# Kernel optimization log

Hardware: AMD Instinct MI355X
Metric: run time of the kernel (lower is better)

The kernel has to match this reference:

```python
import jax, jax.numpy as jnp
import numpy as np
from jax.scipy.linalg import expm as _expm

# --- hyperparameters from transop_cfg ---
LAMBDA_PRIOR = 0.05      # L1 weight (cfg.lambda_prior)
FISTA_ITERS = 20         # cfg.fista_num_iterations
FISTA_LR = 0.01          # FISTA step size
PSI_SCALE = 0.01         # stable operator initialization scale

B, D, K, M, N = 256, 512, 8, 64, 64  # batch, feat dim, blocks, dict size, block dim


def _batch_expm(T):
    # T: [B, K, N, N] -> expm applied to each NxN matrix
    Bk = T.shape[0] * T.shape[1]
    Texp = jax.vmap(_expm)(T.reshape(Bk, N, N))
    return Texp.reshape(T.shape)


def transop_apply(z0, c, psi):
    """z1_hat = expm(sum_m c_m psi[k,m]) @ z0_block, block-diagonal over K blocks.
    z0: [B, D], c: [B, M], psi: [K, M, N, N] -> [B, D]
    """
    z0b = z0.reshape(z0.shape[0], K, N)                  # [B, K, N]
    T = jnp.einsum('bm,kmuv->bkuv', c, psi)              # [B, K, N, N]
    Texp = _batch_expm(T)
    z1b = jnp.einsum('bkuv,bkv->bku', Texp, z0b)         # [B, K, N]
    return z1b.reshape(z0.shape)


def _soft_threshold(x, thr):
    return jnp.sign(x) * jnp.maximum(jnp.abs(x) - thr, 0.0)


def infer_coefficients(z0, z1, psi):
    """FISTA for min_c 0.5*||expm(c.psi) z0 - z1||^2 + lambda*||c||_1."""
    def smooth_loss(c):
        z1_hat = transop_apply(z0, c, psi)
        return 0.5 * jnp.sum((z1_hat - z1) ** 2)

    grad_fn = jax.grad(smooth_loss)

    def body(carry, _):
        c, y, t = carry
        g = grad_fn(y)
        c_new = _soft_threshold(y - FISTA_LR * g, FISTA_LR * LAMBDA_PRIOR)
        t_new = 0.5 * (1.0 + jnp.sqrt(1.0 + 4.0 * t * t))
        y_new = c_new + ((t - 1.0) / t_new) * (c_new - c)
        return (c_new, y_new, t_new), None

    c0 = jnp.zeros((z0.shape[0], M), dtype=z0.dtype)
    (c, _, _), _ = jax.lax.scan(body, (c0, c0, jnp.float32(1.0)), None, length=FISTA_ITERS)
    return c


def setup_inputs() -> dict:
    key = jax.random.key(0)
    k0, k1, kp = jax.random.split(key, 3)
    feature_0 = jax.random.normal(k0, (B, D), dtype=jnp.float32)
    feature_1 = jax.random.normal(k1, (B, D), dtype=jnp.float32)
    psi = PSI_SCALE * jax.random.normal(kp, (K, M, N, N), dtype=jnp.float32)
    return {"feature_0": feature_0, "feature_1": feature_1, "psi": psi}


def reference(feature_0, feature_1, psi):
    z0, z1 = feature_0, feature_1
    # Coefficients inferred on detached features/operators (z0.detach(), psi.float())
    c = infer_coefficients(jax.lax.stop_gradient(z0),
                           jax.lax.stop_gradient(z1),
                           jax.lax.stop_gradient(psi))
    c = jax.lax.stop_gradient(c)
    # Transport: z1_hat = transop(z0, c) with grads flowing to z0 and psi
    z1_hat = transop_apply(z0, c, psi)
    return z1_hat
```

## Files before the change

kernel.cpp:

```cpp
#include <hip/hip_runtime.h>
#include <hip/hip_bf16.h>


typedef __attribute__((ext_vector_type(8))) short bf16x8;
typedef __attribute__((ext_vector_type(4))) float f32x4;
typedef unsigned short ushort_t;
typedef unsigned int uint_t;

__device__ __constant__ float INVF[20] = {
    1.0f, 1.0f, 0.5f, 1.6666666666666666e-1f, 4.1666666666666664e-2f,
    8.333333333333333e-3f, 1.3888888888888889e-3f, 1.984126984126984e-4f,
    2.48015873015873e-5f, 2.7557319223985893e-6f, 2.755731922398589e-7f,
    2.505210838544172e-8f, 2.08767569878681e-9f, 1.6059043836821613e-10f,
    1.1470745597729725e-11f, 7.647163731819816e-13f, 4.779477332387385e-14f,
    2.8114572543455206e-15f, 1.5619206968586225e-16f, 8.22063524662433e-18f};

__device__ __forceinline__ ushort_t f2b(float x) {
    uint_t u = __float_as_uint(x);
    uint_t r = u + 0x7FFFu + ((u >> 16) & 1u);
    return (ushort_t)(r >> 16);
}
__device__ __forceinline__ float b2f(ushort_t h) {
    return __uint_as_float((uint_t)h << 16);
}

__device__ __forceinline__ float qsum4(float s) {
    int a = __builtin_amdgcn_update_dpp(0, __float_as_int(s), 0xB1, 0xF, 0xF, true);
    s += __int_as_float(a);
    int b = __builtin_amdgcn_update_dpp(0, __float_as_int(s), 0x4E, 0xF, 0xF, true);
    s += __int_as_float(b);
    return s;
}

__global__ __launch_bounds__(256) void prep_k(const float* __restrict__ psi,
                                              ushort_t* __restrict__ psiB,
                                              ushort_t* __restrict__ psiT,
                                              uint4* __restrict__ zero_base) {
    if (blockIdx.x < 48)
        zero_base[blockIdx.x * 256 + threadIdx.x] = make_uint4(0, 0, 0, 0);
    int base = blockIdx.x * 2048 + threadIdx.x;
    for (int i = 0; i < 8; ++i) {
        int e = base + i * 256;
        float v = psi[e];
        ushort_t h = f2b(v);
        psiB[e] = h;
        int k = e >> 18;
        int r = e & 262143;
        int m = r >> 12;
        int uv = r & 4095;
        psiT[(size_t)k * 262144 + (size_t)uv * 64 + m] = h;
    }
}

__global__ __launch_bounds__(256) void gemm1_k(const ushort_t* __restrict__ ybf,
                                               const ushort_t* __restrict__ psiT,
                                               ushort_t* __restrict__ Tbf) {
    __shared__ __align__(16) ushort_t Ls[128 * 72];
    int wg = blockIdx.x;
    int j0 = (wg & 511) * 64;
    int bt = wg >> 9;
    int tid = threadIdx.x;
    int wave = tid >> 6, lane = tid & 63;
    int rowi = lane & 15, q = lane >> 4;
    int b0w = bt * 128 + wave * 32;

    f32x4 acc[4][2];
    const f32x4 zero = {0.f, 0.f, 0.f, 0.f};
    for (int ta = 0; ta < 4; ++ta)
        for (int tb = 0; tb < 2; ++tb) acc[ta][tb] = zero;

    for (int ks = 0; ks < 2; ++ks) {
        bf16x8 a[4], bb[2];
        for (int ta = 0; ta < 4; ++ta)
            a[ta] = *(const bf16x8*)(psiT + (size_t)(j0 + ta * 16 + rowi) * 64 +
                                     ks * 32 + q * 8);
        for (int tb = 0; tb < 2; ++tb)
            bb[tb] = *(const bf16x8*)(ybf + (size_t)(b0w + tb * 16 + rowi) * 64 +
                                      ks * 32 + q * 8);
        for (int ta = 0; ta < 4; ++ta)
            for (int tb = 0; tb < 2; ++tb)
                acc[ta][tb] = __builtin_amdgcn_mfma_f32_16x16x32_bf16(
                    a[ta], bb[tb], acc[ta][tb], 0, 0, 0);
    }
    for (int ta = 0; ta < 4; ++ta)
        for (int tb = 0; tb < 2; ++tb) {
            int bl = wave * 32 + tb * 16 + rowi;
            int jl = ta * 16 + q * 4;
            uint_t lo = (uint_t)f2b(acc[ta][tb][0]) | ((uint_t)f2b(acc[ta][tb][1]) << 16);
            uint_t hi = (uint_t)f2b(acc[ta][tb][2]) | ((uint_t)f2b(acc[ta][tb][3]) << 16);
            int idx = bl * 72 + ((((jl >> 3) + 2 * bl) & 7) << 3) + (jl & 7);
            *(uint2*)&Ls[idx] = make_uint2(lo, hi);
        }
    __syncthreads();
    for (int pass = 0; pass < 4; ++pass) {
        int b = pass * 32 + (tid >> 3);
        int ch = tid & 7;
        uint4 v = *(const uint4*)&Ls[b * 72 + ch * 8];
        int x = (ch - 2 * b) & 7;
        *(uint4*)(Tbf + (size_t)(bt * 128 + b) * 32768 + j0 + x * 8) = v;
    }
}

template <int NT>
__global__ __launch_bounds__(256) void krylov_k(ushort_t* __restrict__ Tbf,
                                                const float* __restrict__ z0,
                                                const float* __restrict__ z1,
                                                float* __restrict__ out) {
    __shared__ float V[NT][64];
    __shared__ float U[NT][64];
    __shared__ float zz[64];
    int bid = blockIdx.x;
    int b = bid >> 3, k = bid & 7;
    int tid = threadIdx.x;
    int row = tid >> 2, p = tid & 3, c0 = p * 16;
    bool grad = (out == nullptr);

    const ushort_t* tbase = Tbf + (size_t)bid * 4096;
    float rowT[16];
    {
        uint4 ra = *(const uint4*)(tbase + row * 64 + c0);
        uint4 rb = *(const uint4*)(tbase + row * 64 + c0 + 8);
        uint_t wv[8] = {ra.x, ra.y, ra.z, ra.w, rb.x, rb.y, rb.z, rb.w};
        for (int i = 0; i < 8; ++i) {
            rowT[2 * i]     = __uint_as_float(wv[i] << 16);
            rowT[2 * i + 1] = __uint_as_float(wv[i] & 0xFFFF0000u);
        }
    }
    float colT[16];
    if (grad) {
#pragma unroll
        for (int i = 0; i < 16; ++i) colT[i] = b2f(tbase[(c0 + i) * 64 + row]);
    }
    if (tid < 64) {
        V[0][tid] = z0[(size_t)b * 512 + k * 64 + tid];
        zz[tid]   = z1[(size_t)b * 512 + k * 64 + tid];
    }
    __syncthreads();

    for (int l = 1; l < NT; ++l) {
        const f32x4* vp = (const f32x4*)&V[l - 1][c0];
        f32x4 v0 = vp[0], v1 = vp[1], v2 = vp[2], v3 = vp[3];
        float s0 = 0.f, s1 = 0.f, s2 = 0.f, s3 = 0.f;
#pragma unroll
        for (int i = 0; i < 4; ++i) {
            s0 = fmaf(rowT[i], v0[i], s0);
            s1 = fmaf(rowT[4 + i], v1[i], s1);
            s2 = fmaf(rowT[8 + i], v2[i], s2);
            s3 = fmaf(rowT[12 + i], v3[i], s3);
        }
        float s = qsum4((s0 + s1) + (s2 + s3));
        if (p == 0) V[l][row] = s;
        __syncthreads();
    }

    if (!grad) {
        if (tid < 64) {
            float zh = 0.f;
#pragma unroll
            for (int l = 0; l < NT; ++l) zh = fmaf(INVF[l], V[l][tid], zh);
            out[(size_t)b * 512 + k * 64 + tid] = zh;
        }
        return;
    }

    if (tid < 64) {
        float zh = 0.f;
#pragma unroll
        for (int l = 0; l < NT; ++l) zh = fmaf(INVF[l], V[l][tid], zh);
        U[0][tid] = zh - zz[tid];
    }
    __syncthreads();

    for (int j = 1; j < NT; ++j) {
        const f32x4* up = (const f32x4*)&U[j - 1][c0];
        f32x4 u0 = up[0], u1 = up[1], u2 = up[2], u3 = up[3];
        float s0 = 0.f, s1 = 0.f, s2 = 0.f, s3 = 0.f;
#pragma unroll
        for (int i = 0; i < 4; ++i) {
            s0 = fmaf(colT[i], u0[i], s0);
            s1 = fmaf(colT[4 + i], u1[i], s1);
            s2 = fmaf(colT[8 + i], u2[i], s2);
            s3 = fmaf(colT[12 + i], u3[i], s3);
        }
        float s = qsum4((s0 + s1) + (s2 + s3));
        if (p == 0) U[j][row] = s;
        __syncthreads();
    }

    float W[NT];
#pragma unroll
    for (int l = 0; l < NT; ++l) {
        float w = 0.f;
#pragma unroll
        for (int j = 0; j < NT; ++j) w = fmaf(INVF[j + l + 1], U[j][row], w);
        W[l] = w;
    }
    float o[16];
#pragma unroll
    for (int i = 0; i < 16; ++i) o[i] = 0.f;
#pragma unroll
    for (int l = 0; l < NT; ++l) {
        const f32x4* vp = (const f32x4*)&V[l][c0];
        f32x4 a0 = vp[0], a1 = vp[1], a2 = vp[2], a3 = vp[3];
        float w = W[l];
#pragma unroll
        for (int i = 0; i < 4; ++i) {
            o[i]      = fmaf(w, a0[i], o[i]);
            o[4 + i]  = fmaf(w, a1[i], o[4 + i]);
            o[8 + i]  = fmaf(w, a2[i], o[8 + i]);
            o[12 + i] = fmaf(w, a3[i], o[12 + i]);
        }
    }
    uint_t ow[8];
#pragma unroll
    for (int i = 0; i < 8; ++i)
        ow[i] = (uint_t)f2b(o[2 * i]) | ((uint_t)f2b(o[2 * i + 1]) << 16);
    uint4* op = (uint4*)(Tbf + (size_t)bid * 4096 + row * 64 + c0);
    op[0] = make_uint4(ow[0], ow[1], ow[2], ow[3]);
    op[1] = make_uint4(ow[4], ow[5], ow[6], ow[7]);
}

__global__ __launch_bounds__(256) void gemm2_k(const ushort_t* __restrict__ Obf,
                                               const ushort_t* __restrict__ psiB,
                                               float* __restrict__ gpart) {
    __shared__ __align__(16) float Lg[64 * 68];
    int bt = blockIdx.x & 3;
    int kc = blockIdx.x >> 2;
    int k = kc >> 3;
    int uv0 = (kc & 7) * 512;
    int tid = threadIdx.x, wave = tid >> 6, lane = tid & 63;
    int rowi = lane & 15, q = lane >> 4;

    f32x4 acc[4][4];
    const f32x4 zero = {0.f, 0.f, 0.f, 0.f};
    for (int ta = 0; ta < 4; ++ta)
        for (int tb = 0; tb < 4; ++tb) acc[ta][tb] = zero;

    for (int ks = 0; ks < 4; ++ks) {
        int off = uv0 + wave * 128 + ks * 32 + q * 8;
        bf16x8 a[4], bb[4];
        for (int ta = 0; ta < 4; ++ta)
            a[ta] = *(const bf16x8*)(psiB + (size_t)k * 262144 +
                                     (size_t)(ta * 16 + rowi) * 4096 + off);
        for (int tb = 0; tb < 4; ++tb)
            bb[tb] = *(const bf16x8*)(Obf +
                                      (size_t)(bt * 64 + tb * 16 + rowi) * 32768 +
                                      k * 4096 + off);
        for (int ta = 0; ta < 4; ++ta)
            for (int tb = 0; tb < 4; ++tb)
                acc[ta][tb] = __builtin_amdgcn_mfma_f32_16x16x32_bf16(
                    a[ta], bb[tb], acc[ta][tb], 0, 0, 0);
    }
    for (int w = 0; w < 4; ++w) {
        if (wave == w) {
            for (int ta = 0; ta < 4; ++ta)
                for (int tb = 0; tb < 4; ++tb) {
                    float* dst = &Lg[(tb * 16 + rowi) * 68 + ta * 16 + q * 4];
                    if (w == 0) *(f32x4*)dst = acc[ta][tb];
                    else {
                        f32x4 t = *(const f32x4*)dst;
                        t += acc[ta][tb];
                        *(f32x4*)dst = t;
                    }
                }
        }
        __syncthreads();
    }
    int b = tid >> 2, mq = tid & 3;
    float* gp = gpart + (size_t)kc * 16384 + (size_t)(bt * 64 + b) * 64 + mq * 16;
    const float* lp = &Lg[b * 68 + mq * 16];
    for (int i = 0; i < 4; ++i)
        *(f32x4*)(gp + 4 * i) = *(const f32x4*)(lp + 4 * i);
}

__global__ __launch_bounds__(256) void fista_update(const float* __restrict__ gpart,
                                                    float* __restrict__ cb,
                                                    float* __restrict__ yb,
                                                    ushort_t* __restrict__ cbf,
                                                    ushort_t* __restrict__ ybf,
                                                    int iter) {
    int idx = blockIdx.x * 256 + threadIdx.x;
    float a0 = 0.f, a1 = 0.f, a2 = 0.f, a3 = 0.f;
#pragma unroll
    for (int p = 0; p < 64; p += 4) {
        a0 += gpart[(size_t)p * 16384 + idx];
        a1 += gpart[(size_t)(p + 1) * 16384 + idx];
        a2 += gpart[(size_t)(p + 2) * 16384 + idx];
        a3 += gpart[(size_t)(p + 3) * 16384 + idx];
    }
    float gv = (a0 + a1) + (a2 + a3);
    float t = 1.f;
    for (int s = 0; s < iter; ++s) t = 0.5f * (1.f + sqrtf(1.f + 4.f * t * t));
    float tn = 0.5f * (1.f + sqrtf(1.f + 4.f * t * t));
    float beta = (t - 1.f) / tn;
    float co = cb[idx], yo = yb[idx];
    float a = yo - 0.01f * gv;
    float thr = 0.01f * 0.05f;
    float cn = copysignf(fmaxf(fabsf(a) - thr, 0.f), a);
    float yn = cn + beta * (cn - co);
    cb[idx] = cn;
    yb[idx] = yn;
    cbf[idx] = f2b(cn);
    ybf[idx] = f2b(yn);
}

extern "C" void kernel_launch(void* const* d_in, const int* in_sizes, int n_in,
                              void* d_out, int out_size, void* d_ws, size_t ws_size,
                              hipStream_t stream) {
    const float* z0 = (const float*)d_in[0];
    const float* z1 = (const float*)d_in[1];
    const float* psi = (const float*)d_in[2];
    float* out = (float*)d_out;

    char* w = (char*)d_ws;
    ushort_t* TO    = (ushort_t*)(w);
    ushort_t* psiB  = (ushort_t*)(w + 16777216);
    ushort_t* psiT  = (ushort_t*)(w + 20971520);
    float*    gpart = (float*)(w + 25165824);
    float*    cbuf  = (float*)(w + 29360128);
    float*    ybuf  = (float*)(w + 29425664);
    ushort_t* cbf   = (ushort_t*)(w + 29491200);
    ushort_t* ybf   = (ushort_t*)(w + 29523968);

    prep_k<<<1024, 256, 0, stream>>>(psi, psiB, psiT, (uint4*)(w + 29360128));

    for (int it = 0; it < 20; ++it) {
        gemm1_k<<<1024, 256, 0, stream>>>(ybf, psiT, TO);
        krylov_k<5><<<2048, 256, 0, stream>>>(TO, z0, z1, nullptr);
        gemm2_k<<<256, 256, 0, stream>>>(TO, psiB, gpart);
        fista_update<<<64, 256, 0, stream>>>(gpart, cbuf, ybuf, cbf, ybf, it);
    }

    gemm1_k<<<1024, 256, 0, stream>>>(cbf, psiT, TO);
    krylov_k<8><<<2048, 256, 0, stream>>>(TO, z0, z1, out);
}
```

Baseline: 844.1 us.

## Map one wave per Krylov matrix with register-resident rows and readlane broadcasts

Each 64x64 Krylov matrix is now handled by a single wave instead of a whole 256-thread block. Each lane holds a full row (and column) of T in registers, and vector elements are broadcast with readlane, which removes the shared-memory round trips and block-wide barriers at every Krylov step. The gemm2 reduction also changes: each wave writes its partial tile to its own LDS slice and one sync precedes a combined sum, replacing four serialized sync rounds. The cost is very high register pressure (64-element rowT/colT/o arrays), which lowers occupancy and risks spills, and the strided column load is uncoalesced.

```diff
diff --git a/kernel.cpp b/kernel.cpp
--- a/kernel.cpp
+++ b/kernel.cpp
@@ -23,13 +23,8 @@
 __device__ __forceinline__ float b2f(ushort_t h) {
     return __uint_as_float((uint_t)h << 16);
 }
-
-__device__ __forceinline__ float qsum4(float s) {
-    int a = __builtin_amdgcn_update_dpp(0, __float_as_int(s), 0xB1, 0xF, 0xF, true);
-    s += __int_as_float(a);
-    int b = __builtin_amdgcn_update_dpp(0, __float_as_int(s), 0x4E, 0xF, 0xF, true);
-    s += __int_as_float(b);
-    return s;
+__device__ __forceinline__ float rdlane(float v, int l) {
+    return __int_as_float(__builtin_amdgcn_readlane(__float_as_int(v), l));
 }
 
 __global__ __launch_bounds__(256) void prep_k(const float* __restrict__ psi,
@@ -101,129 +96,112 @@
     }
 }
 
-template <int NT>
+template <int NT, int GRAD>
 __global__ __launch_bounds__(256) void krylov_k(ushort_t* __restrict__ Tbf,
                                                 const float* __restrict__ z0,
                                                 const float* __restrict__ z1,
                                                 float* __restrict__ out) {
-    __shared__ float V[NT][64];
-    __shared__ float U[NT][64];
-    __shared__ float zz[64];
-    int bid = blockIdx.x;
+    int lane = threadIdx.x & 63;
+    int bid = blockIdx.x * 4 + (threadIdx.x >> 6);
     int b = bid >> 3, k = bid & 7;
-    int tid = threadIdx.x;
-    int row = tid >> 2, p = tid & 3, c0 = p * 16;
-    bool grad = (out == nullptr);
-
-    const ushort_t* tbase = Tbf + (size_t)bid * 4096;
-    float rowT[16];
+    ushort_t* tbase = Tbf + (size_t)bid * 4096;
+
+    float rowT[64];
     {
-        uint4 ra = *(const uint4*)(tbase + row * 64 + c0);
-        uint4 rb = *(const uint4*)(tbase + row * 64 + c0 + 8);
-        uint_t wv[8] = {ra.x, ra.y, ra.z, ra.w, rb.x, rb.y, rb.z, rb.w};
-        for (int i = 0; i < 8; ++i) {
-            rowT[2 * i]     = __uint_as_float(wv[i] << 16);
-            rowT[2 * i + 1] = __uint_as_float(wv[i] & 0xFFFF0000u);
-        }
-    }
-    float colT[16];
-    if (grad) {
-#pragma unroll
-        for (int i = 0; i < 16; ++i) colT[i] = b2f(tbase[(c0 + i) * 64 + row]);
-    }
-    if (tid < 64) {
-        V[0][tid] = z0[(size_t)b * 512 + k * 64 + tid];
-        zz[tid]   = z1[(size_t)b * 512 + k * 64 + tid];
-    }
-    __syncthreads();
-
+        const uint4* tp = (const uint4*)(tbase + (size_t)lane * 64);
+#pragma unroll
+        for (int cc = 0; cc < 8; ++cc) {
+            uint4 v = tp[cc];
+            uint_t w[4] = {v.x, v.y, v.z, v.w};
+#pragma unroll
+            for (int i = 0; i < 4; ++i) {
+                rowT[cc * 8 + 2 * i]     = __uint_as_float(w[i] << 16);
+                rowT[cc * 8 + 2 * i + 1] = __uint_as_float(w[i] & 0xFFFF0000u);
+            }
+        }
+    }
+
+    float vs[NT];
+    vs[0] = z0[(size_t)b * 512 + k * 64 + lane];
+#pragma unroll
     for (int l = 1; l < NT; ++l) {
-        const f32x4* vp = (const f32x4*)&V[l - 1][c0];
-        f32x4 v0 = vp[0], v1 = vp[1], v2 = vp[2], v3 = vp[3];
-        float s0 = 0.f, s1 = 0.f, s2 = 0.f, s3 = 0.f;
-#pragma unroll
-        for (int i = 0; i < 4; ++i) {
-            s0 = fmaf(rowT[i], v0[i], s0);
-            s1 = fmaf(rowT[4 + i], v1[i], s1);
-            s2 = fmaf(rowT[8 + i], v2[i], s2);
-            s3 = fmaf(rowT[12 + i], v3[i], s3);
-        }
-        float s = qsum4((s0 + s1) + (s2 + s3));
-        if (p == 0) V[l][row] = s;
-        __syncthreads();
-    }
-
-    if (!grad) {
-        if (tid < 64) {
-            float zh = 0.f;
-#pragma unroll
-            for (int l = 0; l < NT; ++l) zh = fmaf(INVF[l], V[l][tid], zh);
-            out[(size_t)b * 512 + k * 64 + tid] = zh;
-        }
+        float sp = vs[l - 1];
+        float a0 = 0.f, a1 = 0.f, a2 = 0.f, a3 = 0.f;
+#pragma unroll
+        for (int i = 0; i < 64; i += 4) {
+            a0 = fmaf(rowT[i],     rdlane(sp, i),     a0);
+            a1 = fmaf(rowT[i + 1], rdlane(sp, i + 1), a1);
+            a2 = fmaf(rowT[i + 2], rdlane(sp, i + 2), a2);
+            a3 = fmaf(rowT[i + 3], rdlane(sp, i + 3), a3);
+        }
+        vs[l] = (a0 + a1) + (a2 + a3);
+    }
+
+    float zh = 0.f;
+#pragma unroll
+    for (int l = 0; l < NT; ++l) zh = fmaf(INVF[l], vs[l], zh);
+
+    if constexpr (!GRAD) {
+        out[(size_t)b * 512 + k * 64 + lane] = zh;
         return;
-    }
-
-    if (tid < 64) {
-        float zh = 0.f;
-#pragma unroll
-        for (int l = 0; l < NT; ++l) zh = fmaf(INVF[l], V[l][tid], zh);
-        U[0][tid] = zh - zz[tid];
-    }
-    __syncthreads();
-
-    for (int j = 1; j < NT; ++j) {
-        const f32x4* up = (const f32x4*)&U[j - 1][c0];
-        f32x4 u0 = up[0], u1 = up[1], u2 = up[2], u3 = up[3];
-        float s0 = 0.f, s1 = 0.f, s2 = 0.f, s3 = 0.f;
-#pragma unroll
-        for (int i = 0; i < 4; ++i) {
-            s0 = fmaf(colT[i], u0[i], s0);
-            s1 = fmaf(colT[4 + i], u1[i], s1);
-            s2 = fmaf(colT[8 + i], u2[i], s2);
-            s3 = fmaf(colT[12 + i], u3[i], s3);
-        }
-        float s = qsum4((s0 + s1) + (s2 + s3));
-        if (p == 0) U[j][row] = s;
-        __syncthreads();
-    }
-
-    float W[NT];
-#pragma unroll
-    for (int l = 0; l < NT; ++l) {
-        float w = 0.f;
-#pragma unroll
-        for (int j = 0; j < NT; ++j) w = fmaf(INVF[j + l + 1], U[j][row], w);
-        W[l] = w;
-    }
-    float o[16];
-#pragma unroll
-    for (int i = 0; i < 16; ++i) o[i] = 0.f;
-#pragma unroll
-    for (int l = 0; l < NT; ++l) {
-        const f32x4* vp = (const f32x4*)&V[l][c0];
-        f32x4 a0 = vp[0], a1 = vp[1], a2 = vp[2], a3 = vp[3];
-        float w = W[l];
-#pragma unroll
-        for (int i = 0; i < 4; ++i) {
-            o[i]      = fmaf(w, a0[i], o[i]);
-            o[4 + i]  = fmaf(w, a1[i], o[4 + i]);
-            o[8 + i]  = fmaf(w, a2[i], o[8 + i]);
-            o[12 + i] = fmaf(w, a3[i], o[12 + i]);
-        }
-    }
-    uint_t ow[8];
-#pragma unroll
-    for (int i = 0; i < 8; ++i)
-        ow[i] = (uint_t)f2b(o[2 * i]) | ((uint_t)f2b(o[2 * i + 1]) << 16);
-    uint4* op = (uint4*)(Tbf + (size_t)bid * 4096 + row * 64 + c0);
-    op[0] = make_uint4(ow[0], ow[1], ow[2], ow[3]);
-    op[1] = make_uint4(ow[4], ow[5], ow[6], ow[7]);
+    } else {
+        float colT[64];
+#pragma unroll
+        for (int i = 0; i < 64; ++i)
+            colT[i] = b2f(tbase[(size_t)i * 64 + lane]);
+
+        float us[NT];
+        us[0] = zh - z1[(size_t)b * 512 + k * 64 + lane];
+#pragma unroll
+        for (int j = 1; j < NT; ++j) {
+            float sp = us[j - 1];
+            float a0 = 0.f, a1 = 0.f, a2 = 0.f, a3 = 0.f;
+#pragma unroll
+            for (int i = 0; i < 64; i += 4) {
+                a0 = fmaf(colT[i],     rdlane(sp, i),     a0);
+                a1 = fmaf(colT[i + 1], rdlane(sp, i + 1), a1);
+                a2 = fmaf(colT[i + 2], rdlane(sp, i + 2), a2);
+                a3 = fmaf(colT[i + 3], rdlane(sp, i + 3), a3);
+            }
+            us[j] = (a0 + a1) + (a2 + a3);
+        }
+
+        float W[NT];
+#pragma unroll
+        for (int l = 0; l < NT; ++l) {
+            float w = 0.f;
+#pragma unroll
+            for (int j = 0; j < NT; ++j) w = fmaf(INVF[j + l + 1], us[j], w);
+            W[l] = w;
+        }
+
+        float o[64];
+#pragma unroll
+        for (int c = 0; c < 64; ++c) o[c] = 0.f;
+#pragma unroll
+        for (int l = 0; l < NT; ++l) {
+            float wl = W[l];
+#pragma unroll
+            for (int c = 0; c < 64; ++c)
+                o[c] = fmaf(wl, rdlane(vs[l], c), o[c]);
+        }
+
+        uint4* op = (uint4*)(tbase + (size_t)lane * 64);
+#pragma unroll
+        for (int cc = 0; cc < 8; ++cc) {
+            uint_t w0 = (uint_t)f2b(o[cc * 8 + 0]) | ((uint_t)f2b(o[cc * 8 + 1]) << 16);
+            uint_t w1 = (uint_t)f2b(o[cc * 8 + 2]) | ((uint_t)f2b(o[cc * 8 + 3]) << 16);
+            uint_t w2 = (uint_t)f2b(o[cc * 8 + 4]) | ((uint_t)f2b(o[cc * 8 + 5]) << 16);
+            uint_t w3 = (uint_t)f2b(o[cc * 8 + 6]) | ((uint_t)f2b(o[cc * 8 + 7]) << 16);
+            op[cc] = make_uint4(w0, w1, w2, w3);
+        }
+    }
 }
 
 __global__ __launch_bounds__(256) void gemm2_k(const ushort_t* __restrict__ Obf,
                                                const ushort_t* __restrict__ psiB,
                                                float* __restrict__ gpart) {
-    __shared__ __align__(16) float Lg[64 * 68];
+    __shared__ __align__(16) float Lg[4][64 * 68];
     int bt = blockIdx.x & 3;
     int kc = blockIdx.x >> 2;
     int k = kc >> 3;
@@ -251,26 +229,24 @@
                 acc[ta][tb] = __builtin_amdgcn_mfma_f32_16x16x32_bf16(
                     a[ta], bb[tb], acc[ta][tb], 0, 0, 0);
     }
-    for (int w = 0; w < 4; ++w) {
-        if (wave == w) {
-            for (int ta = 0; ta < 4; ++ta)
-                for (int tb = 0; tb < 4; ++tb) {
-                    float* dst = &Lg[(tb * 16 + rowi) * 68 + ta * 16 + q * 4];
-                    if (w == 0) *(f32x4*)dst = acc[ta][tb];
-                    else {
-                        f32x4 t = *(const f32x4*)dst;
-                        t += acc[ta][tb];
-                        *(f32x4*)dst = t;
-                    }
-                }
-        }
-        __syncthreads();
-    }
+    float* lw = &Lg[wave][0];
+    for (int ta = 0; ta < 4; ++ta)
+        for (int tb = 0; tb < 4; ++tb)
+            *(f32x4*)&lw[(tb * 16 + rowi) * 68 + ta * 16 + q * 4] = acc[ta][tb];
+    __syncthreads();
+
     int b = tid >> 2, mq = tid & 3;
+    const float* l0 = &Lg[0][b * 68 + mq * 16];
     float* gp = gpart + (size_t)kc * 16384 + (size_t)(bt * 64 + b) * 64 + mq * 16;
-    const float* lp = &Lg[b * 68 + mq * 16];
-    for (int i = 0; i < 4; ++i)
-        *(f32x4*)(gp + 4 * i) = *(const f32x4*)(lp + 4 * i);
+#pragma unroll
+    for (int i = 0; i < 4; ++i) {
+        f32x4 s0 = *(const f32x4*)(l0 + 4 * i);
+        f32x4 s1 = *(const f32x4*)(l0 + 4352 + 4 * i);
+        f32x4 s2 = *(const f32x4*)(l0 + 8704 + 4 * i);
+        f32x4 s3 = *(const f32x4*)(l0 + 13056 + 4 * i);
+        f32x4 s = (s0 + s1) + (s2 + s3);
+        *(f32x4*)(gp + 4 * i) = s;
+    }
 }
 
 __global__ __launch_bounds__(256) void fista_update(const float* __restrict__ gpart,
@@ -326,11 +302,11 @@
 
     for (int it = 0; it < 20; ++it) {
         gemm1_k<<<1024, 256, 0, stream>>>(ybf, psiT, TO);
-        krylov_k<5><<<2048, 256, 0, stream>>>(TO, z0, z1, nullptr);
+        krylov_k<5, 1><<<512, 256, 0, stream>>>(TO, z0, z1, nullptr);
         gemm2_k<<<256, 256, 0, stream>>>(TO, psiB, gpart);
         fista_update<<<64, 256, 0, stream>>>(gpart, cbuf, ybuf, cbf, ybf, it);
     }
 
     gemm1_k<<<1024, 256, 0, stream>>>(cbf, psiT, TO);
-    krylov_k<8><<<2048, 256, 0, stream>>>(TO, z0, z1, out);
-}
+    krylov_k<8, 0><<<512, 256, 0, stream>>>(TO, z0, z1, out);
+}
```

New measurement: 895.3 us. 6.1% more time.
